# Performance work log

Measured on AMD Instinct MI355X. Metric: run time of the kernel, lower is better.

The kernel has to match this reference:

```python
import jax, jax.numpy as jnp
import numpy as np

N_HEADS = 4
D_K = 64
SCALE = D_K ** (-0.5)


def setup_inputs() -> dict:
    key = jax.random.key(0)
    k1, k2, k3, k4, k5 = jax.random.split(key, 5)
    B, C, H, W = 32, 256, 32, 32
    x = jax.random.normal(k1, (B, C, H, W), dtype=jnp.float32)
    proj_w = jax.random.normal(k2, (N_HEADS * D_K * 3, C), dtype=jnp.float32) * 0.02
    proj_b = jax.random.normal(k3, (N_HEADS * D_K * 3,), dtype=jnp.float32) * 0.02
    out_w = jax.random.normal(k4, (C, N_HEADS * D_K), dtype=jnp.float32) * 0.02
    out_b = jax.random.normal(k5, (C,), dtype=jnp.float32) * 0.02
    return {"x": x, "proj_w": proj_w, "proj_b": proj_b, "out_w": out_w, "out_b": out_b}


def reference(x, proj_w, proj_b, out_w, out_b):
    B, C, H, W = x.shape
    # [B, C, H, W] -> [B, N, C] with N = H*W
    xs = x.reshape(B, C, H * W).transpose(0, 2, 1)
    # fused QKV projection (torch Linear: y = x @ W.T + b)
    qkv = (xs @ proj_w.T + proj_b).reshape(B, H * W, N_HEADS, 3 * D_K)
    q, k, v = jnp.split(qkv, 3, axis=-1)  # each [B, N, h, d_k]
    # full score tensor [B, i, j, h] (the original materializes this)
    scores = jnp.einsum('bihd,bjhd->bijh', q, k) * SCALE
    attn = jax.nn.softmax(scores, axis=2)  # softmax over keys j
    ctx = jnp.einsum('bijh,bjhd->bihd', attn, v).reshape(B, H * W, N_HEADS * D_K)
    out = ctx @ out_w.T + out_b + xs  # output proj + residual (note: GroupNorm unused in orig forward)
    return out.transpose(0, 2, 1).reshape(B, C, H, W)
```

## Files before the change

kernel.cpp:

```cpp
#include <hip/hip_runtime.h>
#include <hip/hip_bf16.h>

#define BB  32
#define CC  256
#define NN  1024
#define NHH 4
#define DKK 64
#define QD  768
#define QSCALE 0.18033688011112042f

typedef __bf16 bf16;
typedef __bf16 bf16x8 __attribute__((ext_vector_type(8)));
typedef float  f32x4  __attribute__((ext_vector_type(4)));
typedef float  f32x16 __attribute__((ext_vector_type(16)));

typedef __attribute__((address_space(1))) const void g_void;
typedef __attribute__((address_space(3))) void l_void;

__global__ __launch_bounds__(256) void k_prep_w(const float* __restrict__ proj_w,
                                                const float* __restrict__ out_w,
                                                bf16* __restrict__ pwt,
                                                bf16* __restrict__ owt) {
    int i = blockIdx.x * 256 + threadIdx.x;
    if (i < QD * CC) {
        int o = i / CC;
        float v = proj_w[i];
        if ((o % 192) < DKK) v *= QSCALE;
        pwt[i] = (bf16)v;
    }
    if (i < CC * CC) {
        owt[i] = (bf16)out_w[i];
    }
}

__global__ __launch_bounds__(256) void k_transpose_x(const float* __restrict__ x,
                                                     bf16* __restrict__ xs) {
    int bid = blockIdx.x;
    int nt = bid & 15;
    int ct = (bid >> 4) & 3;
    int b  = bid >> 6;
    __shared__ float lds[64][65];
    int t = threadIdx.x;
    const float* xp = x + ((size_t)b * CC + ct * 64) * NN + nt * 64;
#pragma unroll
    for (int rep = 0; rep < 16; ++rep) {
        int idx = rep * 256 + t;
        int c = idx >> 6, n = idx & 63;
        lds[c][n] = xp[(size_t)c * NN + n];
    }
    __syncthreads();
    bf16* xo = xs + ((size_t)b * NN + nt * 64) * CC + ct * 64;
#pragma unroll
    for (int rep = 0; rep < 16; ++rep) {
        int idx = rep * 256 + t;
        int c = idx & 63, n = idx >> 6;
        xo[(size_t)n * CC + c] = (bf16)lds[c][n];
    }
}

__global__ __launch_bounds__(256, 4) void k_gemm_qkv(const bf16* __restrict__ A,
                                                     const bf16* __restrict__ Bw,
                                                     const float* __restrict__ bias,
                                                     bf16* __restrict__ qkv,
                                                     bf16* __restrict__ vt) {
    int l = (blockIdx.x & 7) * 192 + (blockIdx.x >> 3);
    int mtile = l / 6, ntile = l % 6;
    int wave = threadIdx.x >> 6, lane = threadIdx.x & 63;
    int wm = wave >> 1, wn = wave & 1;
    int lr = lane & 15, lg = lane >> 4;
    int row0 = mtile * 128, col0 = ntile * 128;

    __shared__ __align__(16) bf16 Abuf[2][4096];
    __shared__ __align__(16) bf16 Bbuf[2][4096];

    int srow = lane >> 2, sc = lane & 3;
    int rA0 = wave * 16 + srow, rA1 = (wave + 4) * 16 + srow;
    const bf16* a0 = A + (size_t)(row0 + rA0) * CC + ((sc ^ ((rA0 >> 1) & 3)) * 8);
    const bf16* a1 = A + (size_t)(row0 + rA1) * CC + ((sc ^ ((rA1 >> 1) & 3)) * 8);
    const bf16* b0 = Bw + (size_t)(col0 + rA0) * CC + ((sc ^ ((rA0 >> 1) & 3)) * 8);
    const bf16* b1 = Bw + (size_t)(col0 + rA1) * CC + ((sc ^ ((rA1 >> 1) & 3)) * 8);

#define STAGE(ks, sel)                                                          \
    do {                                                                        \
        __builtin_amdgcn_global_load_lds((g_void*)(a0 + (ks) * 32),             \
            (l_void*)&Abuf[sel][wave * 512], 16, 0, 0);                         \
        __builtin_amdgcn_global_load_lds((g_void*)(a1 + (ks) * 32),             \
            (l_void*)&Abuf[sel][(wave + 4) * 512], 16, 0, 0);                   \
        __builtin_amdgcn_global_load_lds((g_void*)(b0 + (ks) * 32),             \
            (l_void*)&Bbuf[sel][wave * 512], 16, 0, 0);                         \
        __builtin_amdgcn_global_load_lds((g_void*)(b1 + (ks) * 32),             \
            (l_void*)&Bbuf[sel][(wave + 4) * 512], 16, 0, 0);                   \
    } while (0)

    f32x4 acc[4][4] = {};
    STAGE(0, 0);
    asm volatile("s_waitcnt vmcnt(0)" ::: "memory");
    __builtin_amdgcn_s_barrier();

    int cur = 0;
    for (int ks = 0; ks < 8; ++ks) {
        if (ks + 1 < 8) STAGE(ks + 1, cur ^ 1);
        bf16x8 af[4], bfm[4];
#pragma unroll
        for (int mt = 0; mt < 4; ++mt) {
            int row = wm * 64 + mt * 16 + lr;
            af[mt] = *reinterpret_cast<const bf16x8*>(
                &Abuf[cur][row * 32 + ((lg ^ ((row >> 1) & 3)) * 8)]);
        }
#pragma unroll
        for (int nt = 0; nt < 4; ++nt) {
            int row = wn * 64 + nt * 16 + lr;
            bfm[nt] = *reinterpret_cast<const bf16x8*>(
                &Bbuf[cur][row * 32 + ((lg ^ ((row >> 1) & 3)) * 8)]);
        }
#pragma unroll
        for (int mt = 0; mt < 4; ++mt)
#pragma unroll
            for (int nt = 0; nt < 4; ++nt)
                acc[mt][nt] = __builtin_amdgcn_mfma_f32_16x16x32_bf16(
                    af[mt], bfm[nt], acc[mt][nt], 0, 0, 0);
        asm volatile("s_waitcnt vmcnt(0)" ::: "memory");
        __builtin_amdgcn_s_barrier();
        cur ^= 1;
    }
#undef STAGE

#pragma unroll
    for (int nt = 0; nt < 4; ++nt) {
        int col = col0 + wn * 64 + nt * 16 + lr;
        int sect = col % 192;
        int h = col / 192;
        float bv = bias[col];
        if (sect < DKK) bv *= QSCALE;
#pragma unroll
        for (int mt = 0; mt < 4; ++mt) {
            int rowb = row0 + wm * 64 + mt * 16 + lg * 4;
            if (sect < 128) {
#pragma unroll
                for (int rr = 0; rr < 4; ++rr)
                    qkv[(size_t)(rowb + rr) * QD + col] =
                        (bf16)(acc[mt][nt][rr] + bv);
            } else {
                int d = sect - 128;
                int b = rowb >> 10, n = rowb & 1023;
                int kb = n >> 6, j = n & 63;
                unsigned u0, u1;
                asm("v_cvt_pk_bf16_f32 %0, %1, %2" : "=v"(u0)
                    : "v"(acc[mt][nt][0] + bv), "v"(acc[mt][nt][1] + bv));
                asm("v_cvt_pk_bf16_f32 %0, %1, %2" : "=v"(u1)
                    : "v"(acc[mt][nt][2] + bv), "v"(acc[mt][nt][3] + bv));
                *reinterpret_cast<uint2*>(
                    &vt[(((size_t)(b * NHH + h) * 16 + kb) * 64 + d) * 64 + j]) =
                    make_uint2(u0, u1);
            }
        }
    }
}

__global__ __launch_bounds__(256, 4) void k_attn(const bf16* __restrict__ qkv,
                                                 const bf16* __restrict__ vt,
                                                 bf16* __restrict__ ctx) {
    int bid = blockIdx.x;
    int qt = bid >> 7;
    int bh = bid & 127;
    int b  = bh >> 2;
    int h  = bh & 3;
    int wave = threadIdx.x >> 6, lane = threadIdx.x & 63;
    int lq = lane & 31, hi = lane >> 5;
    int q0 = qt * 128 + wave * 32;

    __shared__ __align__(16) bf16 smem[16384];

    const bf16* qkb = qkv + (size_t)b * NN * QD;
    const bf16* qrow = qkb + (size_t)(q0 + lq) * QD + h * 192 + 8 * hi;
    bf16x8 qf[4];
#pragma unroll
    for (int dk = 0; dk < 4; ++dk)
        qf[dk] = *reinterpret_cast<const bf16x8*>(qrow + 16 * dk);

    const bf16* kglob = qkb + h * 192 + 64;
    const bf16* vtile = vt + (size_t)bh * 16 * 4096;

    int srw = lane >> 3, sch = lane & 7;
    int r0 = wave * 16 + srw;
    int g0 = sch ^ srw ^ ((2 * wave) & 3);
    int g1 = sch ^ srw ^ ((2 * wave + 1) & 3);
    const bf16* kA0 = kglob + (size_t)r0 * QD + g0 * 8;
    const bf16* kA1 = kglob + (size_t)(r0 + 8) * QD + g1 * 8;
    const bf16* vA0 = vtile + r0 * 64 + g0 * 8;
    const bf16* vA1 = vtile + (r0 + 8) * 64 + g1 * 8;

    int swzl = (lq & 7) ^ (lq >> 3);
    int adK[4];
#pragma unroll
    for (int i = 0; i < 4; ++i)
        adK[i] = lq * 64 + (((2 * i) | hi) ^ swzl) * 8;

    f32x16 acc0 = {}, acc1 = {};
    float m = -1e30f, l = 0.f;

#define STAGE(t, BUF)                                                           \
    do {                                                                        \
        size_t ko = (size_t)(t) * 64 * QD;                                      \
        size_t vo = (size_t)(t) * 4096;                                         \
        __builtin_amdgcn_global_load_lds((g_void*)(kA0 + ko),                   \
            (l_void*)&smem[(BUF) * 4096 + wave * 1024], 16, 0, 0);              \
        __builtin_amdgcn_global_load_lds((g_void*)(kA1 + ko),                   \
            (l_void*)&smem[(BUF) * 4096 + wave * 1024 + 512], 16, 0, 0);        \
        __builtin_amdgcn_global_load_lds((g_void*)(vA0 + vo),                   \
            (l_void*)&smem[8192 + (BUF) * 4096 + wave * 1024], 16, 0, 0);       \
        __builtin_amdgcn_global_load_lds((g_void*)(vA1 + vo),                   \
            (l_void*)&smem[8192 + (BUF) * 4096 + wave * 1024 + 512], 16, 0, 0); \
    } while (0)

#define MAX3(a, b, c) fmaxf(fmaxf((a), (b)), (c))

#define COMPUTE(BUF)                                                            \
    do {                                                                        \
        f32x16 s0 = {}, s1 = {};                                                \
        _Pragma("unroll")                                                       \
        for (int dk = 0; dk < 4; ++dk) {                                        \
            bf16x8 kf0 = *reinterpret_cast<const bf16x8*>(                      \
                &smem[adK[dk] + (BUF) * 4096]);                                 \
            bf16x8 kf1 = *reinterpret_cast<const bf16x8*>(                      \
                &smem[adK[dk] + (BUF) * 4096 + 2048]);                          \
            s0 = __builtin_amdgcn_mfma_f32_32x32x16_bf16(kf0, qf[dk], s0, 0, 0, 0); \
            s1 = __builtin_amdgcn_mfma_f32_32x32x16_bf16(kf1, qf[dk], s1, 0, 0, 0); \
        }                                                                       \
        float x0 = MAX3(s0[0], s0[1], s0[2]);                                   \
        float x1 = MAX3(s0[3], s0[4], s0[5]);                                   \
        float x2 = MAX3(s0[6], s0[7], s0[8]);                                   \
        float x3 = MAX3(s0[9], s0[10], s0[11]);                                 \
        float x4 = MAX3(s0[12], s0[13], s0[14]);                                \
        float x5 = MAX3(s1[0], s1[1], s1[2]);                                   \
        float x6 = MAX3(s1[3], s1[4], s1[5]);                                   \
        float x7 = MAX3(s1[6], s1[7], s1[8]);                                   \
        float x8 = MAX3(s1[9], s1[10], s1[11]);                                 \
        float x9 = MAX3(s1[12], s1[13], s1[14]);                                \
        float xa = fmaxf(s0[15], s1[15]);                                       \
        x0 = MAX3(x0, x1, x2);                                                  \
        x3 = MAX3(x3, x4, x5);                                                  \
        x6 = MAX3(x6, x7, x8);                                                  \
        x9 = MAX3(x9, xa, x0);                                                  \
        x3 = fmaxf(x3, x6);                                                     \
        float pm = fmaxf(x9, x3);                                               \
        {                                                                       \
            float a_ = pm, b_ = pm;                                             \
            asm("v_permlane32_swap_b32 %0, %1" : "+v"(a_), "+v"(b_));           \
            pm = fmaxf(a_, b_);                                                 \
        }                                                                       \
        if (__any(pm > m + 8.f)) {                                              \
            float nm = fmaxf(m, pm);                                            \
            float corr = __builtin_amdgcn_exp2f(m - nm);                        \
            l *= corr; acc0 *= corr; acc1 *= corr; m = nm;                      \
        }                                                                       \
        _Pragma("unroll")                                                       \
        for (int i = 0; i < 16; ++i) {                                          \
            s0[i] = __builtin_amdgcn_exp2f(s0[i] - m);                          \
            s1[i] = __builtin_amdgcn_exp2f(s1[i] - m);                          \
        }                                                                       \
        {                                                                       \
            float l0 = (s0[0] + s0[1]) + (s0[2] + s0[3]);                       \
            float l1 = (s0[4] + s0[5]) + (s0[6] + s0[7]);                       \
            float l2 = (s0[8] + s0[9]) + (s0[10] + s0[11]);                     \
            float l3 = (s0[12] + s0[13]) + (s0[14] + s0[15]);                   \
            float l4 = (s1[0] + s1[1]) + (s1[2] + s1[3]);                       \
            float l5 = (s1[4] + s1[5]) + (s1[6] + s1[7]);                       \
            float l6 = (s1[8] + s1[9]) + (s1[10] + s1[11]);                     \
            float l7 = (s1[12] + s1[13]) + (s1[14] + s1[15]);                   \
            l += ((l0 + l1) + (l2 + l3)) + ((l4 + l5) + (l6 + l7));             \
        }                                                                       \
        union { unsigned u[4]; bf16x8 v; } pu[4];                               \
        _Pragma("unroll")                                                       \
        for (int g = 0; g < 2; ++g) {                                           \
            unsigned w0, w1, w2, w3;                                            \
            asm("v_cvt_pk_bf16_f32 %0, %1, %2" : "=v"(w0)                       \
                : "v"(s0[8 * g + 0]), "v"(s0[8 * g + 1]));                      \
            asm("v_cvt_pk_bf16_f32 %0, %1, %2" : "=v"(w1)                       \
                : "v"(s0[8 * g + 2]), "v"(s0[8 * g + 3]));                      \
            asm("v_cvt_pk_bf16_f32 %0, %1, %2" : "=v"(w2)                       \
                : "v"(s0[8 * g + 4]), "v"(s0[8 * g + 5]));                      \
            asm("v_cvt_pk_bf16_f32 %0, %1, %2" : "=v"(w3)                       \
                : "v"(s0[8 * g + 6]), "v"(s0[8 * g + 7]));                      \
            asm("v_permlane32_swap_b32 %0, %1" : "+v"(w0), "+v"(w2));           \
            asm("v_permlane32_swap_b32 %0, %1" : "+v"(w1), "+v"(w3));           \
            pu[g].u[0] = w0; pu[g].u[1] = w1; pu[g].u[2] = w2; pu[g].u[3] = w3; \
            asm("v_cvt_pk_bf16_f32 %0, %1, %2" : "=v"(w0)                       \
                : "v"(s1[8 * g + 0]), "v"(s1[8 * g + 1]));                      \
            asm("v_cvt_pk_bf16_f32 %0, %1, %2" : "=v"(w1)                       \
                : "v"(s1[8 * g + 2]), "v"(s1[8 * g + 3]));                      \
            asm("v_cvt_pk_bf16_f32 %0, %1, %2" : "=v"(w2)                       \
                : "v"(s1[8 * g + 4]), "v"(s1[8 * g + 5]));                      \
            asm("v_cvt_pk_bf16_f32 %0, %1, %2" : "=v"(w3)                       \
                : "v"(s1[8 * g + 6]), "v"(s1[8 * g + 7]));                      \
            asm("v_permlane32_swap_b32 %0, %1" : "+v"(w0), "+v"(w2));           \
            asm("v_permlane32_swap_b32 %0, %1" : "+v"(w1), "+v"(w3));           \
            pu[2 + g].u[0] = w0; pu[2 + g].u[1] = w1;                           \
            pu[2 + g].u[2] = w2; pu[2 + g].u[3] = w3;                           \
        }                                                                       \
        _Pragma("unroll")                                                       \
        for (int kk = 0; kk < 4; ++kk) {                                        \
            bf16x8 v0_ = *reinterpret_cast<const bf16x8*>(                      \
                &smem[adK[kk] + 8192 + (BUF) * 4096]);                          \
            bf16x8 v1_ = *reinterpret_cast<const bf16x8*>(                      \
                &smem[adK[kk] + 8192 + (BUF) * 4096 + 2048]);                   \
            acc0 = __builtin_amdgcn_mfma_f32_32x32x16_bf16(v0_, pu[kk].v, acc0, 0, 0, 0); \
            acc1 = __builtin_amdgcn_mfma_f32_32x32x16_bf16(v1_, pu[kk].v, acc1, 0, 0, 0); \
        }                                                                       \
    } while (0)

    STAGE(0, 0);
    asm volatile("s_waitcnt vmcnt(0)" ::: "memory");
    __builtin_amdgcn_s_barrier();

    for (int t = 0; t < 16; t += 2) {
        STAGE(t + 1, 1);
        COMPUTE(0);
        asm volatile("s_waitcnt vmcnt(0)" ::: "memory");
        __builtin_amdgcn_s_barrier();
        if (t + 2 < 16) STAGE(t + 2, 0);
        COMPUTE(1);
        asm volatile("s_waitcnt vmcnt(0)" ::: "memory");
        __builtin_amdgcn_s_barrier();
    }
#undef STAGE
#undef COMPUTE

    {
        float a = l, b2 = l;
        asm("v_permlane32_swap_b32 %0, %1" : "+v"(a), "+v"(b2));
        l = a + b2;
    }
    float inv = 1.0f / l;

    bf16* tl = &smem[(size_t)wave * 32 * 68];
#pragma unroll
    for (int r = 0; r < 16; ++r) {
        int d = (r & 3) + 8 * (r >> 2) + 4 * hi;
        tl[lq * 68 + d]      = (bf16)(acc0[r] * inv);
        tl[lq * 68 + d + 32] = (bf16)(acc1[r] * inv);
    }
    __syncthreads();
    bf16* cb = ctx + ((size_t)(b * NN + q0)) * 256 + h * 64;
#pragma unroll
    for (int r = 0; r < 4; ++r) {
        int q = 8 * r + (lane >> 3);
        int d0 = (lane & 7) * 8;
        uint2 lo  = *reinterpret_cast<const uint2*>(&tl[q * 68 + d0]);
        uint2 hi2 = *reinterpret_cast<const uint2*>(&tl[q * 68 + d0 + 4]);
        uint4 o4 = make_uint4(lo.x, lo.y, hi2.x, hi2.y);
        *reinterpret_cast<uint4*>(cb + (size_t)q * 256 + d0) = o4;
    }
}

__global__ __launch_bounds__(256, 4) void k_gemm_out(const bf16* __restrict__ A,
                                                     const bf16* __restrict__ Bw,
                                                     const float* __restrict__ bias,
                                                     const float* __restrict__ x,
                                                     float* __restrict__ out) {
    int l = (blockIdx.x & 7) * 128 + (blockIdx.x >> 3);
    int mtile = l >> 2, ntile = l & 3;
    int wave = threadIdx.x >> 6, lane = threadIdx.x & 63;
    int wm = wave >> 1, wn = wave & 1;
    int lr = lane & 15, lg = lane >> 4;
    int row0 = mtile * 128, col0 = ntile * 64;

    __shared__ __align__(16) bf16 Abuf[2][4096];
    __shared__ __align__(16) bf16 Bbuf[2][2048];

    int srow = lane >> 2, sc = lane & 3;
    int rA0 = wave * 16 + srow, rA1 = (wave + 4) * 16 + srow;
    const bf16* a0 = A + (size_t)(row0 + rA0) * CC + ((sc ^ ((rA0 >> 1) & 3)) * 8);
    const bf16* a1 = A + (size_t)(row0 + rA1) * CC + ((sc ^ ((rA1 >> 1) & 3)) * 8);
    const bf16* b0 = Bw + (size_t)(col0 + rA0) * CC + ((sc ^ ((rA0 >> 1) & 3)) * 8);

#define STAGE(ks, sel)                                                          \
    do {                                                                        \
        __builtin_amdgcn_global_load_lds((g_void*)(a0 + (ks) * 32),             \
            (l_void*)&Abuf[sel][wave * 512], 16, 0, 0);                         \
        __builtin_amdgcn_global_load_lds((g_void*)(a1 + (ks) * 32),             \
            (l_void*)&Abuf[sel][(wave + 4) * 512], 16, 0, 0);                   \
        __builtin_amdgcn_global_load_lds((g_void*)(b0 + (ks) * 32),             \
            (l_void*)&Bbuf[sel][wave * 512], 16, 0, 0);                         \
    } while (0)

    f32x4 acc[4][2] = {};
    STAGE(0, 0);
    asm volatile("s_waitcnt vmcnt(0)" ::: "memory");
    __builtin_amdgcn_s_barrier();

    int cur = 0;
    for (int ks = 0; ks < 8; ++ks) {
        if (ks + 1 < 8) STAGE(ks + 1, cur ^ 1);
        bf16x8 af[4], bfm[2];
#pragma unroll
        for (int mt = 0; mt < 4; ++mt) {
            int row = wm * 64 + mt * 16 + lr;
            af[mt] = *reinterpret_cast<const bf16x8*>(
                &Abuf[cur][row * 32 + ((lg ^ ((row >> 1) & 3)) * 8)]);
        }
#pragma unroll
        for (int nt = 0; nt < 2; ++nt) {
            int row = wn * 32 + nt * 16 + lr;
            bfm[nt] = *reinterpret_cast<const bf16x8*>(
                &Bbuf[cur][row * 32 + ((lg ^ ((row >> 1) & 3)) * 8)]);
        }
#pragma unroll
        for (int mt = 0; mt < 4; ++mt)
#pragma unroll
            for (int nt = 0; nt < 2; ++nt)
                acc[mt][nt] = __builtin_amdgcn_mfma_f32_16x16x32_bf16(
                    af[mt], bfm[nt], acc[mt][nt], 0, 0, 0);
        asm volatile("s_waitcnt vmcnt(0)" ::: "memory");
        __builtin_amdgcn_s_barrier();
        cur ^= 1;
    }
#undef STAGE

#pragma unroll
    for (int nt = 0; nt < 2; ++nt) {
        int c = col0 + wn * 32 + nt * 16 + lr;
        float bv = bias[c];
#pragma unroll
        for (int mt = 0; mt < 4; ++mt) {
            int rowb = row0 + wm * 64 + mt * 16 + lg * 4;
            int b = rowb >> 10, n = rowb & 1023;
            size_t o = ((size_t)b * CC + c) * NN + n;
            f32x4 xr = *reinterpret_cast<const f32x4*>(&x[o]);
            f32x4 r = acc[mt][nt] + bv + xr;
            *reinterpret_cast<f32x4*>(&out[o]) = r;
        }
    }
}

extern "C" void kernel_launch(void* const* d_in, const int* in_sizes, int n_in,
                              void* d_out, int out_size, void* d_ws, size_t ws_size,
                              hipStream_t stream) {
    const float* x      = (const float*)d_in[0];
    const float* proj_w = (const float*)d_in[1];
    const float* proj_b = (const float*)d_in[2];
    const float* out_w  = (const float*)d_in[3];
    const float* out_b  = (const float*)d_in[4];
    float* out = (float*)d_out;

    bf16* xs  = (bf16*)d_ws;
    bf16* qkv = xs + (size_t)32768 * 256;
    bf16* vt  = qkv + (size_t)32768 * 768;
    bf16* pwt = vt + (size_t)8388608;
    bf16* owt = pwt + (size_t)768 * 256;
    bf16* ctx = xs;

    k_prep_w     <<<dim3(768),  dim3(256), 0, stream>>>(proj_w, out_w, pwt, owt);
    k_transpose_x<<<dim3(2048), dim3(256), 0, stream>>>(x, xs);
    k_gemm_qkv   <<<dim3(1536), dim3(256), 0, stream>>>(xs, pwt, proj_b, qkv, vt);
    k_attn       <<<dim3(1024), dim3(256), 0, stream>>>(qkv, vt, ctx);
    k_gemm_out   <<<dim3(1024), dim3(256), 0, stream>>>(ctx, owt, out_b, x, out);
}
```

Baseline: 102.8 us.

## Keep two loads in flight with partial vmcnt waits and MFMA priority boosts

Result: slower. 117.6 us (+14.4%).

```diff
diff --git a/kernel.cpp b/kernel.cpp
--- a/kernel.cpp
+++ b/kernel.cpp
@@ -16,6 +16,11 @@
 
 typedef __attribute__((address_space(1))) const void g_void;
 typedef __attribute__((address_space(3))) void l_void;
+
+#define WAITV4 asm volatile("s_waitcnt vmcnt(4)" ::: "memory")
+#define WAITV3 asm volatile("s_waitcnt vmcnt(3)" ::: "memory")
+#define WAITV0 asm volatile("s_waitcnt vmcnt(0)" ::: "memory")
+#define BAR()  __builtin_amdgcn_s_barrier()
 
 __global__ __launch_bounds__(256) void k_prep_w(const float* __restrict__ proj_w,
                                                 const float* __restrict__ out_w,
@@ -80,7 +85,7 @@
     const bf16* b0 = Bw + (size_t)(col0 + rA0) * CC + ((sc ^ ((rA0 >> 1) & 3)) * 8);
     const bf16* b1 = Bw + (size_t)(col0 + rA1) * CC + ((sc ^ ((rA1 >> 1) & 3)) * 8);
 
-#define STAGE(ks, sel)                                                          \
+#define GSTAGE(ks, sel)                                                         \
     do {                                                                        \
         __builtin_amdgcn_global_load_lds((g_void*)(a0 + (ks) * 32),             \
             (l_void*)&Abuf[sel][wave * 512], 16, 0, 0);                         \
@@ -92,38 +97,50 @@
             (l_void*)&Bbuf[sel][(wave + 4) * 512], 16, 0, 0);                   \
     } while (0)
 
+#define GCOMP(BUF)                                                              \
+    do {                                                                        \
+        bf16x8 af[4], bfm[4];                                                   \
+        _Pragma("unroll")                                                       \
+        for (int mt = 0; mt < 4; ++mt) {                                        \
+            int row = wm * 64 + mt * 16 + lr;                                   \
+            af[mt] = *reinterpret_cast<const bf16x8*>(                          \
+                &Abuf[BUF][row * 32 + ((lg ^ ((row >> 1) & 3)) * 8)]);          \
+        }                                                                       \
+        _Pragma("unroll")                                                       \
+        for (int nt = 0; nt < 4; ++nt) {                                        \
+            int row = wn * 64 + nt * 16 + lr;                                   \
+            bfm[nt] = *reinterpret_cast<const bf16x8*>(                         \
+                &Bbuf[BUF][row * 32 + ((lg ^ ((row >> 1) & 3)) * 8)]);          \
+        }                                                                       \
+        _Pragma("unroll")                                                       \
+        for (int mt = 0; mt < 4; ++mt)                                          \
+            _Pragma("unroll")                                                   \
+            for (int nt = 0; nt < 4; ++nt)                                      \
+                acc[mt][nt] = __builtin_amdgcn_mfma_f32_16x16x32_bf16(          \
+                    af[mt], bfm[nt], acc[mt][nt], 0, 0, 0);                     \
+    } while (0)
+
     f32x4 acc[4][4] = {};
-    STAGE(0, 0);
-    asm volatile("s_waitcnt vmcnt(0)" ::: "memory");
-    __builtin_amdgcn_s_barrier();
-
-    int cur = 0;
-    for (int ks = 0; ks < 8; ++ks) {
-        if (ks + 1 < 8) STAGE(ks + 1, cur ^ 1);
-        bf16x8 af[4], bfm[4];
-#pragma unroll
-        for (int mt = 0; mt < 4; ++mt) {
-            int row = wm * 64 + mt * 16 + lr;
-            af[mt] = *reinterpret_cast<const bf16x8*>(
-                &Abuf[cur][row * 32 + ((lg ^ ((row >> 1) & 3)) * 8)]);
-        }
-#pragma unroll
-        for (int nt = 0; nt < 4; ++nt) {
-            int row = wn * 64 + nt * 16 + lr;
-            bfm[nt] = *reinterpret_cast<const bf16x8*>(
-                &Bbuf[cur][row * 32 + ((lg ^ ((row >> 1) & 3)) * 8)]);
-        }
-#pragma unroll
-        for (int mt = 0; mt < 4; ++mt)
-#pragma unroll
-            for (int nt = 0; nt < 4; ++nt)
-                acc[mt][nt] = __builtin_amdgcn_mfma_f32_16x16x32_bf16(
-                    af[mt], bfm[nt], acc[mt][nt], 0, 0, 0);
-        asm volatile("s_waitcnt vmcnt(0)" ::: "memory");
-        __builtin_amdgcn_s_barrier();
-        cur ^= 1;
-    }
-#undef STAGE
+    GSTAGE(0, 0);
+    GSTAGE(1, 1);
+#pragma unroll 1
+    for (int ks = 0; ks < 6; ks += 2) {
+        WAITV4; BAR();
+        GCOMP(0);
+        BAR();
+        GSTAGE(ks + 2, 0);
+        WAITV4; BAR();
+        GCOMP(1);
+        BAR();
+        GSTAGE(ks + 3, 1);
+    }
+    WAITV4; BAR();
+    GCOMP(0);
+    BAR();
+    WAITV0; BAR();
+    GCOMP(1);
+#undef GSTAGE
+#undef GCOMP
 
 #pragma unroll
     for (int nt = 0; nt < 4; ++nt) {
@@ -218,6 +235,7 @@
 #define COMPUTE(BUF)                                                            \
     do {                                                                        \
         f32x16 s0 = {}, s1 = {};                                                \
+        __builtin_amdgcn_s_setprio(1);                                          \
         _Pragma("unroll")                                                       \
         for (int dk = 0; dk < 4; ++dk) {                                        \
             bf16x8 kf0 = *reinterpret_cast<const bf16x8*>(                      \
@@ -227,6 +245,7 @@
             s0 = __builtin_amdgcn_mfma_f32_32x32x16_bf16(kf0, qf[dk], s0, 0, 0, 0); \
             s1 = __builtin_amdgcn_mfma_f32_32x32x16_bf16(kf1, qf[dk], s1, 0, 0, 0); \
         }                                                                       \
+        __builtin_amdgcn_s_setprio(0);                                          \
         float x0 = MAX3(s0[0], s0[1], s0[2]);                                   \
         float x1 = MAX3(s0[3], s0[4], s0[5]);                                   \
         float x2 = MAX3(s0[6], s0[7], s0[8]);                                   \
@@ -298,6 +317,7 @@
             pu[2 + g].u[0] = w0; pu[2 + g].u[1] = w1;                           \
             pu[2 + g].u[2] = w2; pu[2 + g].u[3] = w3;                           \
         }                                                                       \
+        __builtin_amdgcn_s_setprio(1);                                          \
         _Pragma("unroll")                                                       \
         for (int kk = 0; kk < 4; ++kk) {                                        \
             bf16x8 v0_ = *reinterpret_cast<const bf16x8*>(                      \
@@ -307,22 +327,27 @@
             acc0 = __builtin_amdgcn_mfma_f32_32x32x16_bf16(v0_, pu[kk].v, acc0, 0, 0, 0); \
             acc1 = __builtin_amdgcn_mfma_f32_32x32x16_bf16(v1_, pu[kk].v, acc1, 0, 0, 0); \
         }                                                                       \
+        __builtin_amdgcn_s_setprio(0);                                          \
     } while (0)
 
     STAGE(0, 0);
-    asm volatile("s_waitcnt vmcnt(0)" ::: "memory");
-    __builtin_amdgcn_s_barrier();
-
-    for (int t = 0; t < 16; t += 2) {
-        STAGE(t + 1, 1);
+    STAGE(1, 1);
+#pragma unroll 1
+    for (int t = 0; t < 14; t += 2) {
+        WAITV4; BAR();
         COMPUTE(0);
-        asm volatile("s_waitcnt vmcnt(0)" ::: "memory");
-        __builtin_amdgcn_s_barrier();
-        if (t + 2 < 16) STAGE(t + 2, 0);
+        BAR();
+        STAGE(t + 2, 0);
+        WAITV4; BAR();
         COMPUTE(1);
-        asm volatile("s_waitcnt vmcnt(0)" ::: "memory");
-        __builtin_amdgcn_s_barrier();
-    }
+        BAR();
+        STAGE(t + 3, 1);
+    }
+    WAITV4; BAR();
+    COMPUTE(0);
+    BAR();
+    WAITV0; BAR();
+    COMPUTE(1);
 #undef STAGE
 #undef COMPUTE
 
@@ -333,6 +358,7 @@
     }
     float inv = 1.0f / l;
 
+    __syncthreads();
     bf16* tl = &smem[(size_t)wave * 32 * 68];
 #pragma unroll
     for (int r = 0; r < 16; ++r) {
@@ -374,7 +400,7 @@
     const bf16* a1 = A + (size_t)(row0 + rA1) * CC + ((sc ^ ((rA1 >> 1) & 3)) * 8);
     const bf16* b0 = Bw + (size_t)(col0 + rA0) * CC + ((sc ^ ((rA0 >> 1) & 3)) * 8);
 
-#define STAGE(ks, sel)                                                          \
+#define GSTAGE(ks, sel)                                                         \
     do {                                                                        \
         __builtin_amdgcn_global_load_lds((g_void*)(a0 + (ks) * 32),             \
             (l_void*)&Abuf[sel][wave * 512], 16, 0, 0);                         \
@@ -384,38 +410,50 @@
             (l_void*)&Bbuf[sel][wave * 512], 16, 0, 0);                         \
     } while (0)
 
+#define GCOMP(BUF)                                                              \
+    do {                                                                        \
+        bf16x8 af[4], bfm[2];                                                   \
+        _Pragma("unroll")                                                       \
+        for (int mt = 0; mt < 4; ++mt) {                                        \
+            int row = wm * 64 + mt * 16 + lr;                                   \
+            af[mt] = *reinterpret_cast<const bf16x8*>(                          \
+                &Abuf[BUF][row * 32 + ((lg ^ ((row >> 1) & 3)) * 8)]);          \
+        }                                                                       \
+        _Pragma("unroll")                                                       \
+        for (int nt = 0; nt < 2; ++nt) {                                        \
+            int row = wn * 32 + nt * 16 + lr;                                   \
+            bfm[nt] = *reinterpret_cast<const bf16x8*>(                         \
+                &Bbuf[BUF][row * 32 + ((lg ^ ((row >> 1) & 3)) * 8)]);          \
+        }                                                                       \
+        _Pragma("unroll")                                                       \
+        for (int mt = 0; mt < 4; ++mt)                                          \
+            _Pragma("unroll")                                                   \
+            for (int nt = 0; nt < 2; ++nt)                                      \
+                acc[mt][nt] = __builtin_amdgcn_mfma_f32_16x16x32_bf16(          \
+                    af[mt], bfm[nt], acc[mt][nt], 0, 0, 0);                     \
+    } while (0)
+
     f32x4 acc[4][2] = {};
-    STAGE(0, 0);
-    asm volatile("s_waitcnt vmcnt(0)" ::: "memory");
-    __builtin_amdgcn_s_barrier();
-
-    int cur = 0;
-    for (int ks = 0; ks < 8; ++ks) {
-        if (ks + 1 < 8) STAGE(ks + 1, cur ^ 1);
-        bf16x8 af[4], bfm[2];
-#pragma unroll
-        for (int mt = 0; mt < 4; ++mt) {
-            int row = wm * 64 + mt * 16 + lr;
-            af[mt] = *reinterpret_cast<const bf16x8*>(
-                &Abuf[cur][row * 32 + ((lg ^ ((row >> 1) & 3)) * 8)]);
-        }
-#pragma unroll
-        for (int nt = 0; nt < 2; ++nt) {
-            int row = wn * 32 + nt * 16 + lr;
-            bfm[nt] = *reinterpret_cast<const bf16x8*>(
-                &Bbuf[cur][row * 32 + ((lg ^ ((row >> 1) & 3)) * 8)]);
-        }
-#pragma unroll
-        for (int mt = 0; mt < 4; ++mt)
-#pragma unroll
-            for (int nt = 0; nt < 2; ++nt)
-                acc[mt][nt] = __builtin_amdgcn_mfma_f32_16x16x32_bf16(
-                    af[mt], bfm[nt], acc[mt][nt], 0, 0, 0);
-        asm volatile("s_waitcnt vmcnt(0)" ::: "memory");
-        __builtin_amdgcn_s_barrier();
-        cur ^= 1;
-    }
-#undef STAGE
+    GSTAGE(0, 0);
+    GSTAGE(1, 1);
+#pragma unroll 1
+    for (int ks = 0; ks < 6; ks += 2) {
+        WAITV3; BAR();
+        GCOMP(0);
+        BAR();
+        GSTAGE(ks + 2, 0);
+        WAITV3; BAR();
+        GCOMP(1);
+        BAR();
+        GSTAGE(ks + 3, 1);
+    }
+    WAITV3; BAR();
+    GCOMP(0);
+    BAR();
+    WAITV0; BAR();
+    GCOMP(1);
+#undef GSTAGE
+#undef GCOMP
 
 #pragma unroll
     for (int nt = 0; nt < 2; ++nt) {
```
